# Kernel tuning notes

Hardware: AMD Instinct MI355X
Metric: run time of the kernel (lower is better)

Reference implementation:

```python
import jax, jax.numpy as jnp
import numpy as np
from jax import lax

CENSUS_R = 3
EDGE_WEIGHT = 4.0


def _grayscale(img):
    # ITU-R 601 luma, as in tf.image.rgb_to_grayscale used by UnFlow-style census
    w = jnp.array([0.299, 0.587, 0.114], dtype=img.dtype)
    return jnp.einsum('bchw,c->bhw', img, w)[:, None]  # (B,1,H,W)


def _grid(H, W, dtype):
    gy, gx = jnp.meshgrid(jnp.arange(H, dtype=dtype), jnp.arange(W, dtype=dtype), indexing='ij')
    return gy, gx


def _warp_bilinear(img, flow):
    # Resample2d: out(x,y) = img(x + u, y + v), bilinear, clamped at borders.
    B, C, H, W = img.shape
    gy, gx = _grid(H, W, flow.dtype)
    x = gx[None] + flow[:, 0]   # (B,H,W)
    y = gy[None] + flow[:, 1]
    x0 = jnp.floor(x); y0 = jnp.floor(y)
    wx = (x - x0)[:, None]; wy = (y - y0)[:, None]  # (B,1,H,W)
    x0i = jnp.clip(x0.astype(jnp.int32), 0, W - 1)
    x1i = jnp.clip(x0i + 1, 0, W - 1)
    y0i = jnp.clip(y0.astype(jnp.int32), 0, H - 1)
    y1i = jnp.clip(y0i + 1, 0, H - 1)
    flat = img.reshape(B, C, H * W)

    def gather(yi, xi):
        idx = (yi * W + xi).reshape(B, 1, H * W)
        return jnp.take_along_axis(flat, idx, axis=2).reshape(B, C, H, W)

    return (gather(y0i, x0i) * (1.0 - wx) * (1.0 - wy)
            + gather(y0i, x1i) * wx * (1.0 - wy)
            + gather(y1i, x0i) * (1.0 - wx) * wy
            + gather(y1i, x1i) * wx * wy)


def _border_mask(flow):
    # 1 where the flow target lands inside the image, 0 otherwise. (B,1,H,W)
    B, _, H, W = flow.shape
    gy, gx = _grid(H, W, flow.dtype)
    x = gx[None] + flow[:, 0]
    y = gy[None] + flow[:, 1]
    inside = (x >= 0) & (x <= W - 1) & (y >= 0) & (y <= H - 1)
    return inside[:, None].astype(flow.dtype)


def _charbonnier(x, mask=None, alpha=0.45, eps=1e-3):
    err = (x * x + eps * eps) ** alpha
    if mask is not None:
        err = err * mask
    return jnp.sum(err) / x.size


def _census_transform(img, r):
    gray = _grayscale(img) * 255.0
    p = 2 * r + 1
    # identity kernel extracts the (2r+1)^2 neighborhood per pixel
    k = jnp.asarray(np.eye(p * p, dtype=np.float32).reshape(p * p, 1, p, p))
    patches = lax.conv_general_dilated(gray, k, (1, 1), 'SAME',
                                       dimension_numbers=('NCHW', 'OIHW', 'NCHW'))
    d = patches - gray  # (B,p*p,H,W)
    return d / jnp.sqrt(0.81 + d * d)


def _census_loss(img1, img2_warp, mask, r):
    t1 = _census_transform(img1, r)
    t2 = _census_transform(img2_warp, r)
    dist = (t1 - t2) ** 2
    dist = dist / (0.1 + dist)                 # soft hamming per neighbor
    dist = jnp.sum(dist, axis=1, keepdims=True)  # (B,1,H,W)
    B, _, H, W = img1.shape
    inner = jnp.zeros((1, 1, H, W), img1.dtype).at[:, :, r:H - r, r:W - r].set(1.0)
    return _charbonnier(dist, mask * inner)


def _smooth_grad_1st(flow, img, edge_weight):
    img_dx = img[:, :, :, :-1] - img[:, :, :, 1:]
    img_dy = img[:, :, :-1, :] - img[:, :, 1:, :]
    w_x = jnp.exp(-jnp.mean(jnp.abs(img_dx), axis=1, keepdims=True) * edge_weight)
    w_y = jnp.exp(-jnp.mean(jnp.abs(img_dy), axis=1, keepdims=True) * edge_weight)
    f_dx = flow[:, :, :, :-1] - flow[:, :, :, 1:]
    f_dy = flow[:, :, :-1, :] - flow[:, :, 1:, :]
    pen = lambda d: (d * d + 1e-6) ** 0.45  # charbonnier penalty
    return 0.5 * (jnp.mean(w_x * pen(f_dx)) + jnp.mean(w_y * pen(f_dy)))


def setup_inputs() -> dict:
    key = jax.random.key(0)
    k1, k2, k3, k4 = jax.random.split(key, 4)
    B, H, W = 8, 448, 1024
    return {
        'flow1': jax.random.normal(k1, (B, 2, H, W), dtype=jnp.float32),
        'target1': jax.random.normal(k2, (B, 2, H, W), dtype=jnp.float32),
        'input1': jax.random.uniform(k3, (B, 3, H, W), dtype=jnp.float32),
        'input2': jax.random.uniform(k4, (B, 3, H, W), dtype=jnp.float32),
    }


def reference(flow1, target1, input1, input2):
    mask = _border_mask(flow1)
    img2_warp = _warp_bilinear(input2, flow1)
    census = 1.0 * _census_loss(input1, img2_warp, mask, CENSUS_R)
    smooth = 1.0 * _smooth_grad_1st(flow1, input1, EDGE_WEIGHT)
    energy = census + smooth
    epe = jnp.mean(jnp.sqrt(jnp.sum((flow1 - target1) ** 2, axis=1)))
    return (energy, epe)
```

## Files before the change

### kernel.cpp

```cpp
#include <hip/hip_runtime.h>
#include <math.h>

#define BB 8
#define HH 448
#define WW 1024
#define HWSZ (HH*WW)
#define NPIX (BB*HH*WW)
#define CR 3
#define TX 64
#define TY 16
#define HX (TX+2*CR)
#define HXP 72
#define HY (TY+2*CR)
#define NB1 (HH*BB)
#define NB2 (16*28*BB)

__device__ __forceinline__ float pen45(float dd) {
    return __expf(0.45f * __logf(dd));
}


__global__ __launch_bounds__(256) void k_prep(
    const float* __restrict__ flow, const float* __restrict__ target,
    const float* __restrict__ img1, const float* __restrict__ img2,
    float* __restrict__ g1, float* __restrict__ g2,
    float* __restrict__ part_sx, float* __restrict__ part_sy, float* __restrict__ part_epe)
{
    const int tid = threadIdx.x;
    const int y = blockIdx.x;
    const int b = blockIdx.y;
    const int x = tid * 4;
    const int idx = y * WW + x;
    const float* i1r = img1 + (size_t)b * 3 * HWSZ;
    const float* i1g = i1r + HWSZ;
    const float* i1b = i1r + 2 * HWSZ;
    const float* i2r = img2 + (size_t)b * 3 * HWSZ;
    const float* i2g = i2r + HWSZ;
    const float* i2b = i2r + 2 * HWSZ;
    const float* fu = flow + (size_t)b * 2 * HWSZ;
    const float* fv = fu + HWSZ;
    const float* tu = target + (size_t)b * 2 * HWSZ;
    const float* tv = tu + HWSZ;

    float4 a1r = *(const float4*)(i1r + idx);
    float4 a1g = *(const float4*)(i1g + idx);
    float4 a1b = *(const float4*)(i1b + idx);
    float4 a2r = *(const float4*)(i2r + idx);
    float4 a2g = *(const float4*)(i2g + idx);
    float4 a2b = *(const float4*)(i2b + idx);
    float4 au  = *(const float4*)(fu + idx);
    float4 av  = *(const float4*)(fv + idx);
    float4 atu = *(const float4*)(tu + idx);
    float4 atv = *(const float4*)(tv + idx);

    const int nf = (tid == 255) ? 3 : 4;
    float nr = i1r[idx + nf], ng = i1g[idx + nf], nb = i1b[idx + nf];
    float nu = fu[idx + nf],  nv = fv[idx + nf];

    float4 l1, l2;
    l1.x = (0.299f*a1r.x + 0.587f*a1g.x + 0.114f*a1b.x) * 255.0f;
    l1.y = (0.299f*a1r.y + 0.587f*a1g.y + 0.114f*a1b.y) * 255.0f;
    l1.z = (0.299f*a1r.z + 0.587f*a1g.z + 0.114f*a1b.z) * 255.0f;
    l1.w = (0.299f*a1r.w + 0.587f*a1g.w + 0.114f*a1b.w) * 255.0f;
    l2.x = (0.299f*a2r.x + 0.587f*a2g.x + 0.114f*a2b.x) * 255.0f;
    l2.y = (0.299f*a2r.y + 0.587f*a2g.y + 0.114f*a2b.y) * 255.0f;
    l2.z = (0.299f*a2r.z + 0.587f*a2g.z + 0.114f*a2b.z) * 255.0f;
    l2.w = (0.299f*a2r.w + 0.587f*a2g.w + 0.114f*a2b.w) * 255.0f;
    *(float4*)(g1 + (size_t)b * HWSZ + idx) = l1;
    *(float4*)(g2 + (size_t)b * HWSZ + idx) = l2;

    float A1r[5] = {a1r.x, a1r.y, a1r.z, a1r.w, nr};
    float A1g[5] = {a1g.x, a1g.y, a1g.z, a1g.w, ng};
    float A1b[5] = {a1b.x, a1b.y, a1b.z, a1b.w, nb};
    float FU[5]  = {au.x, au.y, au.z, au.w, nu};
    float FV[5]  = {av.x, av.y, av.z, av.w, nv};
    float TU[4]  = {atu.x, atu.y, atu.z, atu.w};
    float TV[4]  = {atv.x, atv.y, atv.z, atv.w};

    float ep = 0.0f, sx = 0.0f, sy = 0.0f;
    #pragma unroll
    for (int k = 0; k < 4; k++) {
        float du = FU[k] - TU[k], dv = FV[k] - TV[k];
        ep += sqrtf(du * du + dv * dv);
        float ad = fabsf(A1r[k] - A1r[k+1]) + fabsf(A1g[k] - A1g[k+1]) + fabsf(A1b[k] - A1b[k+1]);
        float wx = __expf(-(4.0f / 3.0f) * ad);
        float d0 = FU[k] - FU[k+1], d1 = FV[k] - FV[k+1];
        float t = wx * (pen45(fmaf(d0, d0, 1e-6f)) + pen45(fmaf(d1, d1, 1e-6f)));
        if (x + k < WW - 1) sx += t;
    }

    if (y < HH - 1) {
        float4 b1r = *(const float4*)(i1r + idx + WW);
        float4 b1g = *(const float4*)(i1g + idx + WW);
        float4 b1b = *(const float4*)(i1b + idx + WW);
        float4 bu  = *(const float4*)(fu + idx + WW);
        float4 bv  = *(const float4*)(fv + idx + WW);
        float B1r[4] = {b1r.x, b1r.y, b1r.z, b1r.w};
        float B1g[4] = {b1g.x, b1g.y, b1g.z, b1g.w};
        float B1b[4] = {b1b.x, b1b.y, b1b.z, b1b.w};
        float BU[4]  = {bu.x, bu.y, bu.z, bu.w};
        float BV[4]  = {bv.x, bv.y, bv.z, bv.w};
        #pragma unroll
        for (int k = 0; k < 4; k++) {
            float ad = fabsf(A1r[k] - B1r[k]) + fabsf(A1g[k] - B1g[k]) + fabsf(A1b[k] - B1b[k]);
            float wy = __expf(-(4.0f / 3.0f) * ad);
            float d0 = FU[k] - BU[k], d1 = FV[k] - BV[k];
            sy += wy * (pen45(fmaf(d0, d0, 1e-6f)) + pen45(fmaf(d1, d1, 1e-6f)));
        }
    }

    #pragma unroll
    for (int off = 32; off; off >>= 1) {
        ep += __shfl_down(ep, off);
        sx += __shfl_down(sx, off);
        sy += __shfl_down(sy, off);
    }
    __shared__ float red[3][4];
    const int lane = tid & 63, wid = tid >> 6;
    if (lane == 0) { red[0][wid] = sx; red[1][wid] = sy; red[2][wid] = ep; }
    __syncthreads();
    if (tid == 0) {
        const int bid = b * HH + y;
        part_sx[bid]  = red[0][0] + red[0][1] + red[0][2] + red[0][3];
        part_sy[bid]  = red[1][0] + red[1][1] + red[1][2] + red[1][3];
        part_epe[bid] = red[2][0] + red[2][1] + red[2][2] + red[2][3];
    }
}

__global__ __launch_bounds__(256) void k_census(
    const float* __restrict__ flow,
    const float* __restrict__ g1, const float* __restrict__ g2,
    float* __restrict__ part_cen)
{
    __shared__ float t1s[HY][HXP];
    __shared__ float t2s[HY][HXP];
    __shared__ float mks[TY][TX];

    const int b = blockIdx.z;
    const int x0 = CR + blockIdx.x * TX;
    const int y0 = CR + blockIdx.y * TY;
    const float* g1b = g1 + (size_t)b * HWSZ;
    const float* g2b = g2 + (size_t)b * HWSZ;
    const float* fl = flow + (size_t)b * 2 * HWSZ;
    const int tid = threadIdx.x;

    for (int i = tid; i < HY * HX; i += 256) {
        int ly = i / HX, lx = i - ly * HX;
        int gx = x0 - CR + lx; if (gx > WW - 1) gx = WW - 1;
        int gy = y0 - CR + ly; if (gy > HH - 1) gy = HH - 1;
        int gidx = gy * WW + gx;
        t1s[ly][lx] = g1b[gidx];
        float u = fl[gidx], v = fl[HWSZ + gidx];
        float xx = (float)gx + u, yy = (float)gy + v;
        float fx = floorf(xx), fy = floorf(yy);
        float wx = xx - fx, wy = yy - fy;
        int xi0 = (int)fx; xi0 = xi0 < 0 ? 0 : (xi0 > WW - 1 ? WW - 1 : xi0);
        int xi1 = xi0 + 1 > WW - 1 ? WW - 1 : xi0 + 1;
        int yi0 = (int)fy; yi0 = yi0 < 0 ? 0 : (yi0 > HH - 1 ? HH - 1 : yi0);
        int yi1 = yi0 + 1 > HH - 1 ? HH - 1 : yi0 + 1;
        float v00 = g2b[yi0 * WW + xi0], v01 = g2b[yi0 * WW + xi1];
        float v10 = g2b[yi1 * WW + xi0], v11 = g2b[yi1 * WW + xi1];
        t2s[ly][lx] = v00 * ((1.0f - wx) * (1.0f - wy)) + v01 * (wx * (1.0f - wy))
                    + v10 * ((1.0f - wx) * wy) + v11 * (wx * wy);
        if (lx >= CR && lx < CR + TX && ly >= CR && ly < CR + TY)
            mks[ly - CR][lx - CR] = (float)((xx >= 0.0f) && (xx <= (float)(WW - 1)) &&
                                            (yy >= 0.0f) && (yy <= (float)(HH - 1)));
    }
    __syncthreads();

    const int txg = tid & 15;
    const int ty  = tid >> 4;
    const int lxb = txg * 4;
    const int rowc = ty + CR;

    float dist[4] = {0.f, 0.f, 0.f, 0.f};
    float c1[4], c2[4];

#define LOADROW(ROW, V1, V2)                                            \
    float V1[12], V2[12];                                               \
    {                                                                   \
        float4 _a0 = *(const float4*)&t1s[ROW][lxb];                    \
        float4 _a1 = *(const float4*)&t1s[ROW][lxb + 4];                \
        float4 _a2 = *(const float4*)&t1s[ROW][lxb + 8];                \
        float4 _b0 = *(const float4*)&t2s[ROW][lxb];                    \
        float4 _b1 = *(const float4*)&t2s[ROW][lxb + 4];                \
        float4 _b2 = *(const float4*)&t2s[ROW][lxb + 8];                \
        V1[0]=_a0.x; V1[1]=_a0.y; V1[2]=_a0.z; V1[3]=_a0.w;             \
        V1[4]=_a1.x; V1[5]=_a1.y; V1[6]=_a1.z; V1[7]=_a1.w;             \
        V1[8]=_a2.x; V1[9]=_a2.y; V1[10]=_a2.z; V1[11]=_a2.w;           \
        V2[0]=_b0.x; V2[1]=_b0.y; V2[2]=_b0.z; V2[3]=_b0.w;             \
        V2[4]=_b1.x; V2[5]=_b1.y; V2[6]=_b1.z; V2[7]=_b1.w;             \
        V2[8]=_b2.x; V2[9]=_b2.y; V2[10]=_b2.z; V2[11]=_b2.w;           \
    }

#define PAIR(V1, V2, K, DX)                                              \
    {                                                                    \
        float _d1 = V1[3 + (K) + (DX)] - c1[K];                          \
        float _d2 = V2[3 + (K) + (DX)] - c2[K];                          \
        float _u1 = _d1 * __builtin_amdgcn_rsqf(fmaf(_d1, _d1, 0.81f));  \
        float _u2 = _d2 * __builtin_amdgcn_rsqf(fmaf(_d2, _d2, 0.81f));  \
        float _dd = _u1 - _u2;                                           \
        float _s = _dd * _dd;                                            \
        dist[K] = fmaf(_s, __builtin_amdgcn_rcpf(0.1f + _s), dist[K]);   \
    }

    {
        LOADROW(rowc, v1, v2)
        #pragma unroll
        for (int k = 0; k < 4; k++) { c1[k] = v1[3 + k]; c2[k] = v2[3 + k]; }
        #pragma unroll
        for (int k = 0; k < 4; k++) {
            #pragma unroll
            for (int dx = -CR; dx <= CR; dx++) {
                if (dx == 0) continue;
                PAIR(v1, v2, k, dx)
            }
        }
    }
    #pragma unroll
    for (int dyi = 0; dyi < 6; dyi++) {
        const int dy = (dyi < 3) ? (dyi - 3) : (dyi - 2);
        const int row = rowc + dy;
        LOADROW(row, v1, v2)
        #pragma unroll
        for (int k = 0; k < 4; k++) {
            #pragma unroll
            for (int dx = -CR; dx <= CR; dx++) {
                PAIR(v1, v2, k, dx)
            }
        }
    }

    float sum = 0.0f;
    const int cy = y0 + ty;
    const float4 mk = *(const float4*)&mks[ty][lxb];
    const float mka[4] = {mk.x, mk.y, mk.z, mk.w};
    #pragma unroll
    for (int k = 0; k < 4; k++) {
        const int cx = x0 + lxb + k;
        const bool valid = (cx <= WW - 1 - CR) && (cy <= HH - 1 - CR);
        float m = valid ? mka[k] : 0.0f;
        sum += m * pen45(fmaf(dist[k], dist[k], 1e-6f));
    }

    #pragma unroll
    for (int off = 32; off; off >>= 1) sum += __shfl_down(sum, off);
    __shared__ float rs[4];
    if ((tid & 63) == 0) rs[tid >> 6] = sum;
    __syncthreads();
    if (tid == 0) {
        const int bid = (b * gridDim.y + blockIdx.y) * gridDim.x + blockIdx.x;
        part_cen[bid] = rs[0] + rs[1] + rs[2] + rs[3];
    }
#undef LOADROW
#undef PAIR
}

__global__ __launch_bounds__(256) void k_final(
    const float* __restrict__ part_sx, const float* __restrict__ part_sy,
    const float* __restrict__ part_epe, const float* __restrict__ part_cen,
    float* __restrict__ out)
{
    const int tid = threadIdx.x;
    float sx = 0.f, sy = 0.f, ep = 0.f, cn = 0.f;
    for (int i = tid; i < NB1; i += 256) {
        sx += part_sx[i]; sy += part_sy[i]; ep += part_epe[i];
    }
    for (int i = tid; i < NB2; i += 256) cn += part_cen[i];
    #pragma unroll
    for (int off = 32; off; off >>= 1) {
        sx += __shfl_down(sx, off); sy += __shfl_down(sy, off);
        ep += __shfl_down(ep, off); cn += __shfl_down(cn, off);
    }
    __shared__ float r[4][4];
    const int lane = tid & 63, wid = tid >> 6;
    if (lane == 0) { r[0][wid] = sx; r[1][wid] = sy; r[2][wid] = ep; r[3][wid] = cn; }
    __syncthreads();
    if (tid == 0) {
        sx = r[0][0] + r[0][1] + r[0][2] + r[0][3];
        sy = r[1][0] + r[1][1] + r[1][2] + r[1][3];
        ep = r[2][0] + r[2][1] + r[2][2] + r[2][3];
        cn = r[3][0] + r[3][1] + r[3][2] + r[3][3];
        float census = cn / (float)NPIX;
        float mx = sx / (float)((size_t)BB * 2 * HH * (WW - 1));
        float my = sy / (float)((size_t)BB * 2 * (HH - 1) * WW);
        out[0] = census + 0.5f * (mx + my);
        out[1] = ep / (float)NPIX;
    }
}

extern "C" void kernel_launch(void* const* d_in, const int* in_sizes, int n_in,
                              void* d_out, int out_size, void* d_ws, size_t ws_size,
                              hipStream_t stream) {
    const float* flow   = (const float*)d_in[0];
    const float* target = (const float*)d_in[1];
    const float* img1   = (const float*)d_in[2];
    const float* img2   = (const float*)d_in[3];
    float* out = (float*)d_out;

    float* part_sx  = (float*)d_ws;
    float* part_sy  = part_sx + NB1;
    float* part_epe = part_sy + NB1;
    float* part_cen = part_epe + NB1;
    float* g1 = (float*)((char*)d_ws + 65536);
    float* g2 = g1 + (size_t)NPIX;

    dim3 gr1(HH, BB, 1);
    k_prep<<<gr1, dim3(256, 1, 1), 0, stream>>>(flow, target, img1, img2, g1, g2,
                                                part_sx, part_sy, part_epe);

    dim3 gr2((WW - 2 * CR + TX - 1) / TX, (HH - 2 * CR + TY - 1) / TY, BB);
    k_census<<<gr2, dim3(256, 1, 1), 0, stream>>>(flow, g1, g2, part_cen);

    k_final<<<1, dim3(256, 1, 1), 0, stream>>>(part_sx, part_sy, part_epe, part_cen, out);
}
```

Before: 254.2 us.

## Fuse grayscale prep, smoothness and EPE terms into the census tile kernel

```diff
diff --git a/kernel.cpp b/kernel.cpp
--- a/kernel.cpp
+++ b/kernel.cpp
@@ -12,145 +12,53 @@
 #define HX (TX+2*CR)
 #define HXP 72
 #define HY (TY+2*CR)
-#define NB1 (HH*BB)
-#define NB2 (16*28*BB)
+#define NBX 16
+#define NBY 28
+#define NB  (NBX*NBY*BB)
 
 __device__ __forceinline__ float pen45(float dd) {
     return __expf(0.45f * __logf(dd));
 }
 
-
-__global__ __launch_bounds__(256) void k_prep(
+__device__ __forceinline__ float gray3(float r, float g, float b) {
+    return (0.299f * r + 0.587f * g + 0.114f * b) * 255.0f;
+}
+
+
+__global__ __launch_bounds__(256) void k_fused(
     const float* __restrict__ flow, const float* __restrict__ target,
     const float* __restrict__ img1, const float* __restrict__ img2,
-    float* __restrict__ g1, float* __restrict__ g2,
-    float* __restrict__ part_sx, float* __restrict__ part_sy, float* __restrict__ part_epe)
+    float* __restrict__ part)
 {
+    __shared__ float t1s[HY][HXP];
+    __shared__ float t2s[HY][HXP];
+    __shared__ float fus[HY][HXP];
+    __shared__ float fvs[HY][HXP];
+
+    const int b  = blockIdx.z;
+    const int x0 = blockIdx.x * TX;
+    const int y0 = blockIdx.y * TY;
     const int tid = threadIdx.x;
-    const int y = blockIdx.x;
-    const int b = blockIdx.y;
-    const int x = tid * 4;
-    const int idx = y * WW + x;
+
     const float* i1r = img1 + (size_t)b * 3 * HWSZ;
     const float* i1g = i1r + HWSZ;
     const float* i1b = i1r + 2 * HWSZ;
     const float* i2r = img2 + (size_t)b * 3 * HWSZ;
     const float* i2g = i2r + HWSZ;
     const float* i2b = i2r + 2 * HWSZ;
-    const float* fu = flow + (size_t)b * 2 * HWSZ;
-    const float* fv = fu + HWSZ;
-    const float* tu = target + (size_t)b * 2 * HWSZ;
-    const float* tv = tu + HWSZ;
-
-    float4 a1r = *(const float4*)(i1r + idx);
-    float4 a1g = *(const float4*)(i1g + idx);
-    float4 a1b = *(const float4*)(i1b + idx);
-    float4 a2r = *(const float4*)(i2r + idx);
-    float4 a2g = *(const float4*)(i2g + idx);
-    float4 a2b = *(const float4*)(i2b + idx);
-    float4 au  = *(const float4*)(fu + idx);
-    float4 av  = *(const float4*)(fv + idx);
-    float4 atu = *(const float4*)(tu + idx);
-    float4 atv = *(const float4*)(tv + idx);
-
-    const int nf = (tid == 255) ? 3 : 4;
-    float nr = i1r[idx + nf], ng = i1g[idx + nf], nb = i1b[idx + nf];
-    float nu = fu[idx + nf],  nv = fv[idx + nf];
-
-    float4 l1, l2;
-    l1.x = (0.299f*a1r.x + 0.587f*a1g.x + 0.114f*a1b.x) * 255.0f;
-    l1.y = (0.299f*a1r.y + 0.587f*a1g.y + 0.114f*a1b.y) * 255.0f;
-    l1.z = (0.299f*a1r.z + 0.587f*a1g.z + 0.114f*a1b.z) * 255.0f;
-    l1.w = (0.299f*a1r.w + 0.587f*a1g.w + 0.114f*a1b.w) * 255.0f;
-    l2.x = (0.299f*a2r.x + 0.587f*a2g.x + 0.114f*a2b.x) * 255.0f;
-    l2.y = (0.299f*a2r.y + 0.587f*a2g.y + 0.114f*a2b.y) * 255.0f;
-    l2.z = (0.299f*a2r.z + 0.587f*a2g.z + 0.114f*a2b.z) * 255.0f;
-    l2.w = (0.299f*a2r.w + 0.587f*a2g.w + 0.114f*a2b.w) * 255.0f;
-    *(float4*)(g1 + (size_t)b * HWSZ + idx) = l1;
-    *(float4*)(g2 + (size_t)b * HWSZ + idx) = l2;
-
-    float A1r[5] = {a1r.x, a1r.y, a1r.z, a1r.w, nr};
-    float A1g[5] = {a1g.x, a1g.y, a1g.z, a1g.w, ng};
-    float A1b[5] = {a1b.x, a1b.y, a1b.z, a1b.w, nb};
-    float FU[5]  = {au.x, au.y, au.z, au.w, nu};
-    float FV[5]  = {av.x, av.y, av.z, av.w, nv};
-    float TU[4]  = {atu.x, atu.y, atu.z, atu.w};
-    float TV[4]  = {atv.x, atv.y, atv.z, atv.w};
-
-    float ep = 0.0f, sx = 0.0f, sy = 0.0f;
-    #pragma unroll
-    for (int k = 0; k < 4; k++) {
-        float du = FU[k] - TU[k], dv = FV[k] - TV[k];
-        ep += sqrtf(du * du + dv * dv);
-        float ad = fabsf(A1r[k] - A1r[k+1]) + fabsf(A1g[k] - A1g[k+1]) + fabsf(A1b[k] - A1b[k+1]);
-        float wx = __expf(-(4.0f / 3.0f) * ad);
-        float d0 = FU[k] - FU[k+1], d1 = FV[k] - FV[k+1];
-        float t = wx * (pen45(fmaf(d0, d0, 1e-6f)) + pen45(fmaf(d1, d1, 1e-6f)));
-        if (x + k < WW - 1) sx += t;
-    }
-
-    if (y < HH - 1) {
-        float4 b1r = *(const float4*)(i1r + idx + WW);
-        float4 b1g = *(const float4*)(i1g + idx + WW);
-        float4 b1b = *(const float4*)(i1b + idx + WW);
-        float4 bu  = *(const float4*)(fu + idx + WW);
-        float4 bv  = *(const float4*)(fv + idx + WW);
-        float B1r[4] = {b1r.x, b1r.y, b1r.z, b1r.w};
-        float B1g[4] = {b1g.x, b1g.y, b1g.z, b1g.w};
-        float B1b[4] = {b1b.x, b1b.y, b1b.z, b1b.w};
-        float BU[4]  = {bu.x, bu.y, bu.z, bu.w};
-        float BV[4]  = {bv.x, bv.y, bv.z, bv.w};
-        #pragma unroll
-        for (int k = 0; k < 4; k++) {
-            float ad = fabsf(A1r[k] - B1r[k]) + fabsf(A1g[k] - B1g[k]) + fabsf(A1b[k] - B1b[k]);
-            float wy = __expf(-(4.0f / 3.0f) * ad);
-            float d0 = FU[k] - BU[k], d1 = FV[k] - BV[k];
-            sy += wy * (pen45(fmaf(d0, d0, 1e-6f)) + pen45(fmaf(d1, d1, 1e-6f)));
-        }
-    }
-
-    #pragma unroll
-    for (int off = 32; off; off >>= 1) {
-        ep += __shfl_down(ep, off);
-        sx += __shfl_down(sx, off);
-        sy += __shfl_down(sy, off);
-    }
-    __shared__ float red[3][4];
-    const int lane = tid & 63, wid = tid >> 6;
-    if (lane == 0) { red[0][wid] = sx; red[1][wid] = sy; red[2][wid] = ep; }
-    __syncthreads();
-    if (tid == 0) {
-        const int bid = b * HH + y;
-        part_sx[bid]  = red[0][0] + red[0][1] + red[0][2] + red[0][3];
-        part_sy[bid]  = red[1][0] + red[1][1] + red[1][2] + red[1][3];
-        part_epe[bid] = red[2][0] + red[2][1] + red[2][2] + red[2][3];
-    }
-}
-
-__global__ __launch_bounds__(256) void k_census(
-    const float* __restrict__ flow,
-    const float* __restrict__ g1, const float* __restrict__ g2,
-    float* __restrict__ part_cen)
-{
-    __shared__ float t1s[HY][HXP];
-    __shared__ float t2s[HY][HXP];
-    __shared__ float mks[TY][TX];
-
-    const int b = blockIdx.z;
-    const int x0 = CR + blockIdx.x * TX;
-    const int y0 = CR + blockIdx.y * TY;
-    const float* g1b = g1 + (size_t)b * HWSZ;
-    const float* g2b = g2 + (size_t)b * HWSZ;
-    const float* fl = flow + (size_t)b * 2 * HWSZ;
-    const int tid = threadIdx.x;
+    const float* fu  = flow + (size_t)b * 2 * HWSZ;
+    const float* fv  = fu + HWSZ;
+    const float* tu  = target + (size_t)b * 2 * HWSZ;
+    const float* tv  = tu + HWSZ;
 
     for (int i = tid; i < HY * HX; i += 256) {
         int ly = i / HX, lx = i - ly * HX;
-        int gx = x0 - CR + lx; if (gx > WW - 1) gx = WW - 1;
-        int gy = y0 - CR + ly; if (gy > HH - 1) gy = HH - 1;
+        int gx = x0 - CR + lx; gx = gx < 0 ? 0 : (gx > WW - 1 ? WW - 1 : gx);
+        int gy = y0 - CR + ly; gy = gy < 0 ? 0 : (gy > HH - 1 ? HH - 1 : gy);
         int gidx = gy * WW + gx;
-        t1s[ly][lx] = g1b[gidx];
-        float u = fl[gidx], v = fl[HWSZ + gidx];
+        t1s[ly][lx] = gray3(i1r[gidx], i1g[gidx], i1b[gidx]);
+        float u = fu[gidx], v = fv[gidx];
+        fus[ly][lx] = u; fvs[ly][lx] = v;
         float xx = (float)gx + u, yy = (float)gy + v;
         float fx = floorf(xx), fy = floorf(yy);
         float wx = xx - fx, wy = yy - fy;
@@ -158,13 +66,14 @@
         int xi1 = xi0 + 1 > WW - 1 ? WW - 1 : xi0 + 1;
         int yi0 = (int)fy; yi0 = yi0 < 0 ? 0 : (yi0 > HH - 1 ? HH - 1 : yi0);
         int yi1 = yi0 + 1 > HH - 1 ? HH - 1 : yi0 + 1;
-        float v00 = g2b[yi0 * WW + xi0], v01 = g2b[yi0 * WW + xi1];
-        float v10 = g2b[yi1 * WW + xi0], v11 = g2b[yi1 * WW + xi1];
-        t2s[ly][lx] = v00 * ((1.0f - wx) * (1.0f - wy)) + v01 * (wx * (1.0f - wy))
-                    + v10 * ((1.0f - wx) * wy) + v11 * (wx * wy);
-        if (lx >= CR && lx < CR + TX && ly >= CR && ly < CR + TY)
-            mks[ly - CR][lx - CR] = (float)((xx >= 0.0f) && (xx <= (float)(WW - 1)) &&
-                                            (yy >= 0.0f) && (yy <= (float)(HH - 1)));
+        int i00 = yi0 * WW + xi0, i01 = yi0 * WW + xi1;
+        int i10 = yi1 * WW + xi0, i11 = yi1 * WW + xi1;
+        float g00 = gray3(i2r[i00], i2g[i00], i2b[i00]);
+        float g01 = gray3(i2r[i01], i2g[i01], i2b[i01]);
+        float g10 = gray3(i2r[i10], i2g[i10], i2b[i10]);
+        float g11 = gray3(i2r[i11], i2g[i11], i2b[i11]);
+        t2s[ly][lx] = g00 * ((1.0f - wx) * (1.0f - wy)) + g01 * (wx * (1.0f - wy))
+                    + g10 * ((1.0f - wx) * wy) + g11 * (wx * wy);
     }
     __syncthreads();
 
@@ -230,57 +139,126 @@
             }
         }
     }
-
-    float sum = 0.0f;
+#undef LOADROW
+#undef PAIR
+
     const int cy = y0 + ty;
-    const float4 mk = *(const float4*)&mks[ty][lxb];
-    const float mka[4] = {mk.x, mk.y, mk.z, mk.w};
+    const int cxb = x0 + lxb;
+
+    float s_cen = 0.0f;
     #pragma unroll
     for (int k = 0; k < 4; k++) {
-        const int cx = x0 + lxb + k;
-        const bool valid = (cx <= WW - 1 - CR) && (cy <= HH - 1 - CR);
-        float m = valid ? mka[k] : 0.0f;
-        sum += m * pen45(fmaf(dist[k], dist[k], 1e-6f));
-    }
-
-    #pragma unroll
-    for (int off = 32; off; off >>= 1) sum += __shfl_down(sum, off);
-    __shared__ float rs[4];
-    if ((tid & 63) == 0) rs[tid >> 6] = sum;
+        const int cx = cxb + k;
+        const bool validc = (cx >= CR) && (cx <= WW - 1 - CR) && (cy >= CR) && (cy <= HH - 1 - CR);
+        float u = fus[rowc][lxb + CR + k], v = fvs[rowc][lxb + CR + k];
+        float xx = (float)cx + u, yy = (float)cy + v;
+        const bool inside = (xx >= 0.0f) && (xx <= (float)(WW - 1)) &&
+                            (yy >= 0.0f) && (yy <= (float)(HH - 1));
+        if (validc && inside) s_cen += pen45(fmaf(dist[k], dist[k], 1e-6f));
+    }
+
+    const int gidx  = cy * WW + cxb;
+    const int xnext = (cxb + 4 > WW - 1) ? (WW - 1) : (cxb + 4);
+    const int gidxn = cy * WW + xnext;
+    const int ydn   = (cy + 1 > HH - 1) ? (HH - 1) : (cy + 1);
+    const int gidxd = ydn * WW + cxb;
+
+    float4 r4 = *(const float4*)(i1r + gidx);
+    float4 g4 = *(const float4*)(i1g + gidx);
+    float4 b4 = *(const float4*)(i1b + gidx);
+    float rn = i1r[gidxn], gn = i1g[gidxn], bn = i1b[gidxn];
+    float4 u4 = *(const float4*)(fu + gidx);
+    float4 v4 = *(const float4*)(fv + gidx);
+    float un = fu[gidxn], vn = fv[gidxn];
+    float4 tu4 = *(const float4*)(tu + gidx);
+    float4 tv4 = *(const float4*)(tv + gidx);
+
+    float R[5] = {r4.x, r4.y, r4.z, r4.w, rn};
+    float G[5] = {g4.x, g4.y, g4.z, g4.w, gn};
+    float Bc[5] = {b4.x, b4.y, b4.z, b4.w, bn};
+    float U[5] = {u4.x, u4.y, u4.z, u4.w, un};
+    float V[5] = {v4.x, v4.y, v4.z, v4.w, vn};
+    float TU[4] = {tu4.x, tu4.y, tu4.z, tu4.w};
+    float TV[4] = {tv4.x, tv4.y, tv4.z, tv4.w};
+
+    float s_ep = 0.0f, s_sx = 0.0f, s_sy = 0.0f;
+    #pragma unroll
+    for (int k = 0; k < 4; k++) {
+        float du = U[k] - TU[k], dv = V[k] - TV[k];
+        s_ep += sqrtf(du * du + dv * dv);
+        if (cxb + k < WW - 1) {
+            float ad = fabsf(R[k] - R[k+1]) + fabsf(G[k] - G[k+1]) + fabsf(Bc[k] - Bc[k+1]);
+            float wx = __expf(-(4.0f / 3.0f) * ad);
+            float d0 = U[k] - U[k+1], d1 = V[k] - V[k+1];
+            s_sx += wx * (pen45(fmaf(d0, d0, 1e-6f)) + pen45(fmaf(d1, d1, 1e-6f)));
+        }
+    }
+
+    if (cy < HH - 1) {
+        float4 rd = *(const float4*)(i1r + gidxd);
+        float4 gd = *(const float4*)(i1g + gidxd);
+        float4 bd = *(const float4*)(i1b + gidxd);
+        float4 ud = *(const float4*)(fu + gidxd);
+        float4 vd = *(const float4*)(fv + gidxd);
+        float RD[4] = {rd.x, rd.y, rd.z, rd.w};
+        float GD[4] = {gd.x, gd.y, gd.z, gd.w};
+        float BD[4] = {bd.x, bd.y, bd.z, bd.w};
+        float UD[4] = {ud.x, ud.y, ud.z, ud.w};
+        float VD[4] = {vd.x, vd.y, vd.z, vd.w};
+        #pragma unroll
+        for (int k = 0; k < 4; k++) {
+            float ad = fabsf(R[k] - RD[k]) + fabsf(G[k] - GD[k]) + fabsf(Bc[k] - BD[k]);
+            float wy = __expf(-(4.0f / 3.0f) * ad);
+            float d0 = U[k] - UD[k], d1 = V[k] - VD[k];
+            s_sy += wy * (pen45(fmaf(d0, d0, 1e-6f)) + pen45(fmaf(d1, d1, 1e-6f)));
+        }
+    }
+
+    #pragma unroll
+    for (int off = 32; off; off >>= 1) {
+        s_cen += __shfl_down(s_cen, off);
+        s_sx  += __shfl_down(s_sx, off);
+        s_sy  += __shfl_down(s_sy, off);
+        s_ep  += __shfl_down(s_ep, off);
+    }
+    __shared__ float red[4][4];
+    const int lane = tid & 63, wid = tid >> 6;
+    if (lane == 0) { red[0][wid] = s_cen; red[1][wid] = s_sx; red[2][wid] = s_sy; red[3][wid] = s_ep; }
     __syncthreads();
     if (tid == 0) {
-        const int bid = (b * gridDim.y + blockIdx.y) * gridDim.x + blockIdx.x;
-        part_cen[bid] = rs[0] + rs[1] + rs[2] + rs[3];
-    }
-#undef LOADROW
-#undef PAIR
+        const int bid = (b * NBY + blockIdx.y) * NBX + blockIdx.x;
+        part[bid]           = red[0][0] + red[0][1] + red[0][2] + red[0][3];
+        part[NB + bid]      = red[1][0] + red[1][1] + red[1][2] + red[1][3];
+        part[2 * NB + bid]  = red[2][0] + red[2][1] + red[2][2] + red[2][3];
+        part[3 * NB + bid]  = red[3][0] + red[3][1] + red[3][2] + red[3][3];
+    }
 }
 
 __global__ __launch_bounds__(256) void k_final(
-    const float* __restrict__ part_sx, const float* __restrict__ part_sy,
-    const float* __restrict__ part_epe, const float* __restrict__ part_cen,
-    float* __restrict__ out)
+    const float* __restrict__ part, float* __restrict__ out)
 {
     const int tid = threadIdx.x;
-    float sx = 0.f, sy = 0.f, ep = 0.f, cn = 0.f;
-    for (int i = tid; i < NB1; i += 256) {
-        sx += part_sx[i]; sy += part_sy[i]; ep += part_epe[i];
-    }
-    for (int i = tid; i < NB2; i += 256) cn += part_cen[i];
+    float cn = 0.f, sx = 0.f, sy = 0.f, ep = 0.f;
+    for (int i = tid; i < NB; i += 256) {
+        cn += part[i];
+        sx += part[NB + i];
+        sy += part[2 * NB + i];
+        ep += part[3 * NB + i];
+    }
     #pragma unroll
     for (int off = 32; off; off >>= 1) {
-        sx += __shfl_down(sx, off); sy += __shfl_down(sy, off);
-        ep += __shfl_down(ep, off); cn += __shfl_down(cn, off);
+        cn += __shfl_down(cn, off); sx += __shfl_down(sx, off);
+        sy += __shfl_down(sy, off); ep += __shfl_down(ep, off);
     }
     __shared__ float r[4][4];
     const int lane = tid & 63, wid = tid >> 6;
-    if (lane == 0) { r[0][wid] = sx; r[1][wid] = sy; r[2][wid] = ep; r[3][wid] = cn; }
+    if (lane == 0) { r[0][wid] = cn; r[1][wid] = sx; r[2][wid] = sy; r[3][wid] = ep; }
     __syncthreads();
     if (tid == 0) {
-        sx = r[0][0] + r[0][1] + r[0][2] + r[0][3];
-        sy = r[1][0] + r[1][1] + r[1][2] + r[1][3];
-        ep = r[2][0] + r[2][1] + r[2][2] + r[2][3];
-        cn = r[3][0] + r[3][1] + r[3][2] + r[3][3];
+        cn = r[0][0] + r[0][1] + r[0][2] + r[0][3];
+        sx = r[1][0] + r[1][1] + r[1][2] + r[1][3];
+        sy = r[2][0] + r[2][1] + r[2][2] + r[2][3];
+        ep = r[3][0] + r[3][1] + r[3][2] + r[3][3];
         float census = cn / (float)NPIX;
         float mx = sx / (float)((size_t)BB * 2 * HH * (WW - 1));
         float my = sy / (float)((size_t)BB * 2 * (HH - 1) * WW);
@@ -296,21 +274,10 @@
     const float* target = (const float*)d_in[1];
     const float* img1   = (const float*)d_in[2];
     const float* img2   = (const float*)d_in[3];
-    float* out = (float*)d_out;
-
-    float* part_sx  = (float*)d_ws;
-    float* part_sy  = part_sx + NB1;
-    float* part_epe = part_sy + NB1;
-    float* part_cen = part_epe + NB1;
-    float* g1 = (float*)((char*)d_ws + 65536);
-    float* g2 = g1 + (size_t)NPIX;
-
-    dim3 gr1(HH, BB, 1);
-    k_prep<<<gr1, dim3(256, 1, 1), 0, stream>>>(flow, target, img1, img2, g1, g2,
-                                                part_sx, part_sy, part_epe);
-
-    dim3 gr2((WW - 2 * CR + TX - 1) / TX, (HH - 2 * CR + TY - 1) / TY, BB);
-    k_census<<<gr2, dim3(256, 1, 1), 0, stream>>>(flow, g1, g2, part_cen);
-
-    k_final<<<1, dim3(256, 1, 1), 0, stream>>>(part_sx, part_sy, part_epe, part_cen, out);
-}
+    float* out  = (float*)d_out;
+    float* part = (float*)d_ws;
+
+    dim3 gr(NBX, NBY, BB);
+    k_fused<<<gr, dim3(256, 1, 1), 0, stream>>>(flow, target, img1, img2, part);
+    k_final<<<1, dim3(256, 1, 1), 0, stream>>>(part, out);
+}
```

Result: slower. 295.8 us (+16.4%).
